# Performance work log

Measured on AMD Instinct MI355X. Metric: run time of the kernel, lower is better.

The kernel has to match this reference:

```python
import jax, jax.numpy as jnp
from jax import lax
import numpy as np

B, S, G = 16, 384, 384
N = S + G
E_CHAR, D = 100, 128
H = D // 2              # LSTM hidden per direction
NHEAD, NHID = 4, 64
T = 21                  # crf_input_dim = label_alphabet.size() + 1
START, STOP = T - 2, T - 1
ALPHA = 0.2
CHAR_V, GAZ_V = 8000, 100000
NEG = -9e15             # pyGAT masked_fill value


def setup_inputs():
    key = jax.random.key(0)
    ks = jax.random.split(key, 20)
    f32 = jnp.float32
    def nrm(k, shape, s=0.05):
        return (jax.random.normal(k, shape) * s).astype(f32)
    eye = jnp.eye(N, dtype=bool)
    def adj(k):
        return ((jax.random.uniform(k, (B, N, N)) < 0.1) | eye[None]).astype(jnp.int32)
    return dict(
        batch_char=jax.random.randint(ks[0], (B, S), 0, CHAR_V),
        batch_len=jnp.full((B,), S, jnp.int32),
        gaz_list=jax.random.randint(ks[1], (B, G), 0, GAZ_V),
        t_graph=adj(ks[2]), c_graph=adj(ks[3]), l_graph=adj(ks[4]),
        mask=jnp.ones((B, S), jnp.int32),
        char_table=nrm(ks[5], (CHAR_V, E_CHAR)),
        gaz_table=nrm(ks[6], (GAZ_V, D)),
        w_ih_f=nrm(ks[7], (4 * H, E_CHAR)), w_hh_f=nrm(ks[8], (4 * H, H)),
        b_f=jnp.zeros((4 * H,), f32),
        w_ih_b=nrm(ks[9], (4 * H, E_CHAR)), w_hh_b=nrm(ks[10], (4 * H, H)),
        b_b=jnp.zeros((4 * H,), f32),
        h2h_W=nrm(ks[11], (T, D)), h2h_b=jnp.zeros((T,), f32),
        gat_Wh=nrm(ks[12], (3, NHEAD, D, NHID)),
        gat_ah=nrm(ks[13], (3, NHEAD, 2 * NHID)),
        gat_Wo=nrm(ks[14], (3, NHEAD * NHID, T)),
        gat_ao=nrm(ks[15], (3, 2 * T)),
        fuse_w=jnp.ones((4,), f32),
        transitions=nrm(ks[16], (T, T)),
    )


def _lstm_dir(x, w_ih, w_hh, b, reverse):
    # x: [B,S,E]; torch gate order i,f,g,o
    Bb = x.shape[0]
    Hh = w_hh.shape[1]
    xw = jnp.einsum('bse,ge->bsg', x, w_ih) + b
    def step(carry, xt):
        h, c = carry
        g = xt + h @ w_hh.T
        i, f, gg, o = jnp.split(g, 4, axis=-1)
        c = jax.nn.sigmoid(f) * c + jax.nn.sigmoid(i) * jnp.tanh(gg)
        h = jax.nn.sigmoid(o) * jnp.tanh(c)
        return (h, c), h
    h0 = jnp.zeros((Bb, Hh), x.dtype)
    _, hs = lax.scan(step, (h0, h0), xw.swapaxes(0, 1), reverse=reverse)
    return hs.swapaxes(0, 1)


def _gat_layer(x, adj, W, a, concat):
    # pyGAT batched layer: e_ij = LeakyReLU(a . [Wh_i || Wh_j]), masked softmax over j
    h = jnp.einsum('bnd,df->bnf', x, W)
    F_ = W.shape[1]
    f1 = h @ a[:F_]           # [B,N]
    f2 = h @ a[F_:]
    e = jax.nn.leaky_relu(f1[:, :, None] + f2[:, None, :], negative_slope=ALPHA)
    e = jnp.where(adj > 0, e, NEG)
    att = jax.nn.softmax(e, axis=-1)
    out = jnp.einsum('bij,bjf->bif', att, h)
    return jax.nn.elu(out) if concat else out


def _gat(x, adj, Wh, ah, Wo, ao):
    heads = jax.vmap(lambda W, a: _gat_layer(x, adj, W, a, True))(Wh, ah)  # [H,B,N,F]
    hcat = jnp.moveaxis(heads, 0, 2).reshape(x.shape[0], x.shape[1], -1)
    return jax.nn.elu(_gat_layer(hcat, adj, Wo, ao, False))


def _crf_feature(batch_char, gaz_list, graphs, char_table, gaz_table,
                 w_ih_f, w_hh_f, b_f, w_ih_b, w_hh_b, b_b, h2h_W, h2h_b,
                 gat_Wh, gat_ah, gat_Wo, gat_ao, fuse_w):
    emb = char_table[batch_char]                      # [B,S,E_CHAR]
    hf = _lstm_dir(emb, w_ih_f, w_hh_f, b_f, False)
    hb = _lstm_dir(emb, w_ih_b, w_hh_b, b_b, True)
    lstm_feat = jnp.concatenate([hf, hb], axis=-1)    # [B,S,D]
    gaz_feat = gaz_table[gaz_list]                    # [B,G,D]
    gat_in = jnp.concatenate([lstm_feat, gaz_feat], axis=1)  # [B,N,D]
    gat_outs = [_gat(gat_in, adj, gat_Wh[k], gat_ah[k], gat_Wo[k], gat_ao[k])[:, :S]
                for k, adj in enumerate(graphs)]
    lstm_proj = lstm_feat @ h2h_W.T + h2h_b           # [B,S,T]
    return (fuse_w[0] * lstm_proj + fuse_w[1] * gat_outs[0]
            + fuse_w[2] * gat_outs[1] + fuse_w[3] * gat_outs[2])


def _viterbi(feats, transitions, mask):
    Bb, Ss, Tt = feats.shape
    ids = jnp.arange(Tt)
    part0 = feats[:, 0, :] + transitions[START][None, :]
    def step(part, inp):
        feat_t, m_t = inp
        cur = part[:, :, None] + transitions[None] + feat_t[:, None, :]  # [B,prev,cur]
        new = cur.max(axis=1)
        bp = cur.argmax(axis=1)
        m = (m_t > 0)[:, None]
        return jnp.where(m, new, part), jnp.where(m, bp, ids[None, :])
    part, bps = lax.scan(step, part0,
                         (feats[:, 1:].swapaxes(0, 1), mask[:, 1:].swapaxes(0, 1)))
    last_tag = jnp.argmax(part + transitions[:, STOP][None, :], axis=1)
    def back(tag, bp):
        prev = jnp.take_along_axis(bp, tag[:, None], axis=1)[:, 0]
        return prev, prev
    _, prevs = lax.scan(back, last_tag, bps, reverse=True)   # prevs[j] = tag at time j
    return jnp.concatenate([prevs.swapaxes(0, 1), last_tag[:, None]], axis=1)


def reference(batch_char, batch_len, gaz_list, t_graph, c_graph, l_graph, mask,
              char_table, gaz_table, w_ih_f, w_hh_f, b_f, w_ih_b, w_hh_b, b_b,
              h2h_W, h2h_b, gat_Wh, gat_ah, gat_Wo, gat_ao, fuse_w, transitions):
    # batch_len is all == S (mask all ones), so packed BiLSTM == plain BiLSTM
    feats = _crf_feature(batch_char, gaz_list, (t_graph, c_graph, l_graph),
                         char_table, gaz_table, w_ih_f, w_hh_f, b_f,
                         w_ih_b, w_hh_b, b_b, h2h_W, h2h_b,
                         gat_Wh, gat_ah, gat_Wo, gat_ao, fuse_w)
    return _viterbi(feats, transitions, mask)
```

## Files before the change

kernel.cpp:

```cpp
#include <hip/hip_runtime.h>
#include <hip/hip_bf16.h>
#include <cstdint>
#include <cstddef>

#define BB 16
#define SS 384
#define GG 384
#define NN 768
#define DD 128
#define EC 100
#define TT 21
#define NHEADS 4
#define BN (BB*NN)
#define BS (BB*SS)

__device__ __forceinline__ float rdlane(float v, int l) {
    return __int_as_float(__builtin_amdgcn_readlane(__float_as_int(v), l));
}
__device__ __forceinline__ float sigf(float x) { return 1.0f / (1.0f + __expf(-x)); }
__device__ __forceinline__ float wred_max(float v) {
    #pragma unroll
    for (int o = 32; o > 0; o >>= 1) v = fmaxf(v, __shfl_xor(v, o));
    return v;
}
__device__ __forceinline__ float wred_sum(float v) {
    #pragma unroll
    for (int o = 32; o > 0; o >>= 1) v += __shfl_xor(v, o);
    return v;
}

__global__ __launch_bounds__(256) void k_xw(
    const int* __restrict__ batch_char, const float* __restrict__ char_table,
    const float* __restrict__ w_ih_f, const float* __restrict__ b_f,
    const float* __restrict__ w_ih_b, const float* __restrict__ b_b,
    float* __restrict__ xw_f, float* __restrict__ xw_b)
{
    __shared__ float At[EC * 68];
    __shared__ float Bt[EC * 68];
    __shared__ int   chs[64];
    const int tid = threadIdx.x;
    const int rt  = blockIdx.x;
    const int ot  = blockIdx.y;
    const int dir = ot >> 2, gt = ot & 3;
    const float* wih  = dir ? w_ih_b : w_ih_f;
    const float* bias = dir ? b_b    : b_f;
    float*       out  = dir ? xw_b   : xw_f;

    if (tid < 64) chs[tid] = batch_char[rt * 64 + tid];
    __syncthreads();
    for (int idx = tid; idx < 64 * EC; idx += 256) {
        int r = idx / EC, e = idx - r * EC;
        At[e * 68 + r] = char_table[(size_t)chs[r] * EC + e];
        Bt[e * 68 + r] = wih[(size_t)(gt * 64 + r) * EC + e];
    }
    __syncthreads();

    const int ty = tid >> 4, tx = tid & 15;
    const int r0 = ty * 4, c0 = tx * 4;
    float acc[4][4] = {};
    #pragma unroll 4
    for (int e = 0; e < EC; ++e) {
        float4 a = *(const float4*)&At[e * 68 + r0];
        float4 bv = *(const float4*)&Bt[e * 68 + c0];
        float av[4] = {a.x, a.y, a.z, a.w};
        float bb[4] = {bv.x, bv.y, bv.z, bv.w};
        #pragma unroll
        for (int i = 0; i < 4; ++i)
            #pragma unroll
            for (int j = 0; j < 4; ++j) acc[i][j] = fmaf(av[i], bb[j], acc[i][j]);
    }
    #pragma unroll
    for (int i = 0; i < 4; ++i) {
        int row = rt * 64 + r0 + i;
        int gc  = gt * 64 + c0;
        float4 o;
        o.x = acc[i][0] + bias[gc + 0];
        o.y = acc[i][1] + bias[gc + 1];
        o.z = acc[i][2] + bias[gc + 2];
        o.w = acc[i][3] + bias[gc + 3];
        *(float4*)&out[(size_t)row * 256 + gc] = o;
    }
}

__global__ __launch_bounds__(256) void k_gaz(
    const int* __restrict__ gaz_list, const float* __restrict__ gaz_table,
    float* __restrict__ gat_in)
{
    int idx = blockIdx.x * 256 + threadIdx.x;
    int d = idx & 127;
    int rest = idx >> 7;
    int g = rest % GG;
    int b = rest / GG;
    float v = gaz_table[(size_t)gaz_list[b * GG + g] * DD + d];
    gat_in[((size_t)b * NN + SS + g) * DD + d] = v;
}

__global__ __launch_bounds__(256) void k_lstm(
    const float* __restrict__ xw_f, const float* __restrict__ xw_b,
    const float* __restrict__ w_hh_f, const float* __restrict__ w_hh_b,
    float* __restrict__ gat_in)
{
    __shared__ float pre[2][256];
    const int tid = threadIdx.x, wave = tid >> 6, lane = tid & 63;
    const int b = blockIdx.x >> 1, dir = blockIdx.x & 1;
    const float* xw = (dir ? xw_b : xw_f) + (size_t)b * SS * 256;
    const float* wrow = (dir ? w_hh_b : w_hh_f) + (size_t)tid * 64;
    float w[64];
    #pragma unroll
    for (int q = 0; q < 16; ++q) {
        float4 v = *(const float4*)&wrow[q * 4];
        w[q * 4 + 0] = v.x; w[q * 4 + 1] = v.y; w[q * 4 + 2] = v.z; w[q * 4 + 3] = v.w;
    }
    float h = 0.f, c = 0.f;
    int buf = 0;
    for (int tt = 0; tt < SS; ++tt) {
        const int t = dir ? (SS - 1 - tt) : tt;
        float pv = xw[t * 256 + tid];
        #pragma unroll
        for (int j = 0; j < 64; ++j) pv = fmaf(rdlane(h, j), w[j], pv);
        pre[buf][lane * 4 + wave] = pv;
        __syncthreads();
        float4 g4 = *(const float4*)&pre[buf][lane * 4];
        float nc = sigf(g4.y) * c + sigf(g4.x) * tanhf(g4.z);
        float nh = sigf(g4.w) * tanhf(nc);
        c = nc; h = nh;
        if (wave == 0) gat_in[((size_t)b * NN + t) * DD + dir * 64 + lane] = h;
        buf ^= 1;
    }
}

__global__ __launch_bounds__(256) void k_p1(
    const float* __restrict__ gat_in, const float* __restrict__ gat_Wh,
    const float* __restrict__ gat_ah, int k,
    float* __restrict__ h1, float* __restrict__ f1g, float* __restrict__ f2g)
{
    __shared__ float At[64 * 68];
    __shared__ float Bt[64 * 68];
    __shared__ float sf1[64], sf2[64];
    const int tid = threadIdx.x;
    const int rt = blockIdx.x, hd = blockIdx.y;
    if (tid < 64) { sf1[tid] = 0.f; sf2[tid] = 0.f; }
    const float* W = gat_Wh + ((size_t)(k * NHEADS + hd)) * DD * 64;
    const int ty = tid >> 4, tx = tid & 15;
    const int r0 = ty * 4, c0 = tx * 4;
    float acc[4][4] = {};
    for (int ph = 0; ph < 2; ++ph) {
        __syncthreads();
        for (int idx = tid; idx < 64 * 64; idx += 256) {
            int r = idx >> 6, e = idx & 63;
            At[e * 68 + r] = gat_in[((size_t)(rt * 64 + r)) * DD + ph * 64 + e];
            int e2 = idx >> 6, f = idx & 63;
            Bt[e2 * 68 + f] = W[(size_t)(ph * 64 + e2) * 64 + f];
        }
        __syncthreads();
        #pragma unroll 4
        for (int e = 0; e < 64; ++e) {
            float4 a = *(const float4*)&At[e * 68 + r0];
            float4 bv = *(const float4*)&Bt[e * 68 + c0];
            float av[4] = {a.x, a.y, a.z, a.w};
            float bb[4] = {bv.x, bv.y, bv.z, bv.w};
            #pragma unroll
            for (int i = 0; i < 4; ++i)
                #pragma unroll
                for (int j = 0; j < 4; ++j) acc[i][j] = fmaf(av[i], bb[j], acc[i][j]);
        }
    }
    const float* ah = gat_ah + (size_t)(k * NHEADS + hd) * 128;
    float a1[4], a2[4];
    #pragma unroll
    for (int j = 0; j < 4; ++j) { a1[j] = ah[c0 + j]; a2[j] = ah[64 + c0 + j]; }
    #pragma unroll
    for (int i = 0; i < 4; ++i) {
        int n = rt * 64 + r0 + i;
        float4 o = make_float4(acc[i][0], acc[i][1], acc[i][2], acc[i][3]);
        *(float4*)&h1[((size_t)n * NHEADS + hd) * 64 + c0] = o;
        float p1 = acc[i][0] * a1[0] + acc[i][1] * a1[1] + acc[i][2] * a1[2] + acc[i][3] * a1[3];
        float p2 = acc[i][0] * a2[0] + acc[i][1] * a2[1] + acc[i][2] * a2[2] + acc[i][3] * a2[3];
        atomicAdd(&sf1[r0 + i], p1);
        atomicAdd(&sf2[r0 + i], p2);
    }
    __syncthreads();
    if (tid < 64) {
        f1g[hd * BN + rt * 64 + tid] = sf1[tid];
        f2g[hd * BN + rt * 64 + tid] = sf2[tid];
    }
}

__global__ __launch_bounds__(256) void k_attn1(
    const int* __restrict__ adj, const float* __restrict__ h1,
    const float* __restrict__ f1g, const float* __restrict__ f2g,
    float* __restrict__ out1, unsigned long long* __restrict__ packed)
{
    __shared__ int   nbr[NN];
    __shared__ float ep[NHEADS][NN];
    __shared__ int   cnt;
    const int tid = threadIdx.x, wave = tid >> 6, lane = tid & 63;
    const int n = blockIdx.x;
    const int b = n / NN;
    if (tid == 0) cnt = 0;
    __syncthreads();
    #pragma unroll
    for (int it = 0; it < 3; ++it) {
        int j = it * 256 + tid;
        int a = adj[(size_t)n * NN + j];
        unsigned long long m = __ballot(a > 0);
        if (lane == 0) packed[(size_t)n * 12 + it * 4 + wave] = m;
        if (a > 0) { int p = atomicAdd(&cnt, 1); nbr[p] = j; }
    }
    __syncthreads();
    const int C = cnt;
    const int hd = wave;
    const float f1 = f1g[hd * BN + n];
    const float* f2p = f2g + hd * BN + b * NN;
    float mx = -3.0e38f;
    for (int t = lane; t < C; t += 64) {
        int j = nbr[t];
        float e = f1 + f2p[j];
        e = (e >= 0.f) ? e : 0.2f * e;
        ep[hd][t] = e;
        mx = fmaxf(mx, e);
    }
    mx = wred_max(mx);
    float sum = 0.f;
    for (int t = lane; t < C; t += 64) {
        float p = __expf(ep[hd][t] - mx);
        ep[hd][t] = p;
        sum += p;
    }
    sum = wred_sum(sum);
    const float* hb = h1 + (size_t)b * NN * (NHEADS * 64) + hd * 64 + lane;
    float acc = 0.f;
    #pragma unroll 4
    for (int t = 0; t < C; ++t) {
        float p = ep[hd][t];
        int j = nbr[t];
        acc = fmaf(p, hb[(size_t)j * (NHEADS * 64)], acc);
    }
    float r = acc / sum;
    r = (r > 0.f) ? r : expm1f(r);
    out1[(size_t)n * 256 + hd * 64 + lane] = r;
}

__global__ __launch_bounds__(256) void k_p2(
    const float* __restrict__ out1, const float* __restrict__ gat_Wo,
    const float* __restrict__ gat_ao, int k,
    float* __restrict__ h2, float* __restrict__ f1o, float* __restrict__ f2o)
{
    __shared__ float ld[12 * 256];
    __shared__ float lf1[12], lf2[12];
    const int tid = threadIdx.x;
    const int blk = blockIdx.x;
    if (tid < 12) { lf1[tid] = 0.f; lf2[tid] = 0.f; }
    for (int idx = tid; idx < 12 * 256; idx += 256)
        ld[idx] = out1[(size_t)blk * 12 * 256 + idx];
    __syncthreads();
    if (tid < 252) {
        const int r = tid / TT, c = tid - r * TT;
        const float* Wo = gat_Wo + (size_t)k * 256 * TT;
        const float4* row4 = (const float4*)&ld[r * 256];
        float acc = 0.f;
        #pragma unroll 8
        for (int q4 = 0; q4 < 64; ++q4) {
            float4 v = row4[q4];
            int q = q4 * 4;
            acc = fmaf(v.x, Wo[(q + 0) * TT + c], acc);
            acc = fmaf(v.y, Wo[(q + 1) * TT + c], acc);
            acc = fmaf(v.z, Wo[(q + 2) * TT + c], acc);
            acc = fmaf(v.w, Wo[(q + 3) * TT + c], acc);
        }
        const int n = blk * 12 + r;
        h2[(size_t)n * TT + c] = acc;
        const float* ao = gat_ao + k * 2 * TT;
        atomicAdd(&lf1[r], acc * ao[c]);
        atomicAdd(&lf2[r], acc * ao[TT + c]);
    }
    __syncthreads();
    if (tid < 12) {
        f1o[blk * 12 + tid] = lf1[tid];
        f2o[blk * 12 + tid] = lf2[tid];
    }
}

__global__ __launch_bounds__(64) void k_attn2(
    const unsigned long long* __restrict__ packed,
    const float* __restrict__ h2, const float* __restrict__ f1o,
    const float* __restrict__ f2o, float* __restrict__ out2k)
{
    __shared__ int   nbr[NN];
    __shared__ float ep[NN];
    const int lane = threadIdx.x;
    const int blk = blockIdx.x;
    const int b = blk / SS, s = blk - b * SS;
    const int n = b * NN + s;
    unsigned long long w64 = (lane < 12) ? packed[(size_t)n * 12 + lane] : 0ULL;
    int pc = __popcll(w64);
    int inc = pc;
    #pragma unroll
    for (int d = 1; d < 16; d <<= 1) {
        int t = __shfl_up(inc, d, 16);
        if ((lane & 15) >= d) inc += t;
    }
    const int C = __shfl(inc, 11);
    int off = inc - pc;
    while (w64) {
        int bit = __builtin_ctzll(w64);
        nbr[off++] = lane * 64 + bit;
        w64 &= w64 - 1;
    }
    __syncthreads();
    const float f1 = f1o[n];
    const float* f2p = f2o + b * NN;
    float mx = -3.0e38f;
    for (int t = lane; t < C; t += 64) {
        int j = nbr[t];
        float e = f1 + f2p[j];
        e = (e >= 0.f) ? e : 0.2f * e;
        ep[t] = e;
        mx = fmaxf(mx, e);
    }
    mx = wred_max(mx);
    float sum = 0.f;
    for (int t = lane; t < C; t += 64) {
        float p = __expf(ep[t] - mx);
        ep[t] = p;
        sum += p;
    }
    sum = wred_sum(sum);
    float acc = 0.f;
    const float* h2b = h2 + (size_t)b * NN * TT + ((lane < TT) ? lane : 0);
    #pragma unroll 4
    for (int t = 0; t < C; ++t) {
        float p = ep[t];
        int j = nbr[t];
        acc = fmaf(p, h2b[(size_t)j * TT], acc);
    }
    if (lane < TT) {
        float r = acc / sum;
        r = (r > 0.f) ? r : expm1f(r);
        out2k[(size_t)blk * TT + lane] = r;
    }
}

__global__ __launch_bounds__(64) void k_fuse(
    const float* __restrict__ gat_in, const float* __restrict__ h2h_W,
    const float* __restrict__ h2h_b, const float* __restrict__ fuse_w,
    const float* __restrict__ out2, float* __restrict__ feats)
{
    __shared__ float row[DD];
    const int lane = threadIdx.x;
    const int blk = blockIdx.x;
    const int b = blk / SS, s = blk - b * SS;
    const float* src = gat_in + ((size_t)b * NN + s) * DD;
    row[lane] = src[lane];
    row[lane + 64] = src[lane + 64];
    __syncthreads();
    if (lane < TT) {
        float acc = h2h_b[lane];
        const float4* w4 = (const float4*)&h2h_W[lane * DD];
        const float4* r4 = (const float4*)row;
        #pragma unroll 8
        for (int d4 = 0; d4 < 32; ++d4) {
            float4 w = w4[d4]; float4 v = r4[d4];
            acc = fmaf(w.x, v.x, acc); acc = fmaf(w.y, v.y, acc);
            acc = fmaf(w.z, v.z, acc); acc = fmaf(w.w, v.w, acc);
        }
        size_t o = (size_t)blk * TT + lane;
        feats[o] = fuse_w[0] * acc + fuse_w[1] * out2[o]
                 + fuse_w[2] * out2[(size_t)BS * TT + o]
                 + fuse_w[3] * out2[2 * (size_t)BS * TT + o];
    }
}

__global__ __launch_bounds__(64) void k_vit(
    const float* __restrict__ feats, const float* __restrict__ trans,
    int* __restrict__ out)
{
    __shared__ float part[24];
    __shared__ unsigned char bp[SS - 1][24];
    const int lane = threadIdx.x;
    const int b = blockIdx.x;
    const int pg = lane / TT;
    const int c = lane - pg * TT;
    const bool act = (pg < 3);
    const int p0 = pg * 7;
    float tc[7];
    if (act) {
        #pragma unroll
        for (int u = 0; u < 7; ++u) tc[u] = trans[(p0 + u) * TT + c];
    }
    if (lane < TT) part[lane] = feats[((size_t)b * SS) * TT + lane] + trans[19 * TT + lane];
    if (lane >= TT && lane < 24) part[lane] = -3.0e38f;
    __syncthreads();
    for (int t = 1; t < SS; ++t) {
        float best = -3.0e38f; int bi = 0;
        if (act) {
            #pragma unroll
            for (int u = 0; u < 7; ++u) {
                float v = part[p0 + u] + tc[u];
                if (v > best) { best = v; bi = p0 + u; }
            }
        }
        float bv1 = __shfl(best, lane + 21);
        int   bi1 = __shfl(bi,   lane + 21);
        float bv2 = __shfl(best, lane + 42);
        int   bi2 = __shfl(bi,   lane + 42);
        if (lane < TT) {
            if (bv1 > best) { best = bv1; bi = bi1; }
            if (bv2 > best) { best = bv2; bi = bi2; }
            bp[t - 1][lane] = (unsigned char)bi;
            part[lane] = best + feats[((size_t)b * SS + t) * TT + lane];
        }
        __syncthreads();
    }
    float fv = (lane < TT) ? part[lane] + trans[lane * TT + 20] : -3.0e38f;
    int fi = (lane < TT) ? lane : 0;
    #pragma unroll
    for (int o = 32; o > 0; o >>= 1) {
        float ov = __shfl_xor(fv, o);
        int oi = __shfl_xor(fi, o);
        if (ov > fv || (ov == fv && oi < fi)) { fv = ov; fi = oi; }
    }
    __syncthreads();
    if (lane == 0) {
        int cur = fi;
        out[b * SS + SS - 1] = cur;
        for (int u = SS - 2; u >= 0; --u) {
            cur = bp[u][cur];
            out[b * SS + u] = cur;
        }
    }
}

extern "C" void kernel_launch(void* const* d_in, const int* in_sizes, int n_in,
                              void* d_out, int out_size, void* d_ws, size_t ws_size,
                              hipStream_t stream) {
    (void)in_sizes; (void)n_in; (void)out_size; (void)ws_size;
    const int*   batch_char = (const int*)d_in[0];
    const int*   gaz_list   = (const int*)d_in[2];
    const int*   graphs[3]  = {(const int*)d_in[3], (const int*)d_in[4], (const int*)d_in[5]};
    const float* char_table = (const float*)d_in[7];
    const float* gaz_table  = (const float*)d_in[8];
    const float* w_ih_f = (const float*)d_in[9];
    const float* w_hh_f = (const float*)d_in[10];
    const float* b_f    = (const float*)d_in[11];
    const float* w_ih_b = (const float*)d_in[12];
    const float* w_hh_b = (const float*)d_in[13];
    const float* b_b    = (const float*)d_in[14];
    const float* h2h_W  = (const float*)d_in[15];
    const float* h2h_b  = (const float*)d_in[16];
    const float* gat_Wh = (const float*)d_in[17];
    const float* gat_ah = (const float*)d_in[18];
    const float* gat_Wo = (const float*)d_in[19];
    const float* gat_ao = (const float*)d_in[20];
    const float* fuse_w = (const float*)d_in[21];
    const float* trans  = (const float*)d_in[22];

    float* ws = (float*)d_ws;
    float* gat_in = ws;
    float* xw_f   = gat_in + 1572864;
    float* xw_b   = xw_f   + 1572864;
    float* h1     = xw_b   + 1572864;
    float* out1   = h1     + 3145728;
    float* h2     = out1   + 3145728;
    float* f1g    = h2     + 258048;
    float* f2g    = f1g    + 49152;
    float* f1o    = f2g    + 49152;
    float* f2o    = f1o    + 12288;
    float* out2   = f2o    + 12288;
    float* feats  = out2   + 387072;
    unsigned long long* packed = (unsigned long long*)(feats + 129024);

    k_xw<<<dim3(96, 8), 256, 0, stream>>>(batch_char, char_table, w_ih_f, b_f,
                                          w_ih_b, b_b, xw_f, xw_b);
    k_gaz<<<3072, 256, 0, stream>>>(gaz_list, gaz_table, gat_in);
    k_lstm<<<32, 256, 0, stream>>>(xw_f, xw_b, w_hh_f, w_hh_b, gat_in);
    for (int k = 0; k < 3; ++k) {
        k_p1<<<dim3(192, 4), 256, 0, stream>>>(gat_in, gat_Wh, gat_ah, k, h1, f1g, f2g);
        k_attn1<<<BN, 256, 0, stream>>>(graphs[k], h1, f1g, f2g, out1, packed);
        k_p2<<<1024, 256, 0, stream>>>(out1, gat_Wo, gat_ao, k, h2, f1o, f2o);
        k_attn2<<<BS, 64, 0, stream>>>(packed, h2, f1o, f2o, out2 + (size_t)k * BS * TT);
    }
    k_fuse<<<BS, 64, 0, stream>>>(gat_in, h2h_W, h2h_b, fuse_w, out2, feats);
    k_vit<<<BB, 64, 0, stream>>>(feats, trans, (int*)d_out);
}
```

Before: 1.039 ms.

## Prefetch LSTM inputs, split FMA chains, deterministic neighbor lists, unroll attention gathers

In the LSTM recurrence, the next step's input projection is prefetched, the 64-term recurrent dot product is split into four independent accumulators, gate values are read from a contiguous shared layout, and tanhf is replaced by an exp-based fast tanh. The GAT attention kernels now build neighbor lists from ballot masks with a prefix sum instead of shared atomics. Their gather-accumulate loops use four independent accumulators to raise memory-level parallelism. The aim is to shorten the serial latency chain in the LSTM and the atomic contention and dependent loads in attention. In exchange, the fast tanh and the reordered sums change floating-point rounding slightly.

```diff
diff --git a/kernel.cpp b/kernel.cpp
--- a/kernel.cpp
+++ b/kernel.cpp
@@ -18,6 +18,9 @@
     return __int_as_float(__builtin_amdgcn_readlane(__float_as_int(v), l));
 }
 __device__ __forceinline__ float sigf(float x) { return 1.0f / (1.0f + __expf(-x)); }
+__device__ __forceinline__ float tanh_fast(float x) {
+    return 1.0f - 2.0f / (__expf(2.0f * x) + 1.0f);
+}
 __device__ __forceinline__ float wred_max(float v) {
     #pragma unroll
     for (int o = 32; o > 0; o >>= 1) v = fmaxf(v, __shfl_xor(v, o));
@@ -113,18 +116,30 @@
     }
     float h = 0.f, c = 0.f;
     int buf = 0;
+    float xv = xw[(dir ? (SS - 1) : 0) * 256 + tid];
     for (int tt = 0; tt < SS; ++tt) {
         const int t = dir ? (SS - 1 - tt) : tt;
-        float pv = xw[t * 256 + tid];
+        const int tn = dir ? (t - 1) : (t + 1);
+        float xnext = (tt + 1 < SS) ? xw[tn * 256 + tid] : 0.f;
+        float a0 = xv, a1 = 0.f, a2 = 0.f, a3 = 0.f;
         #pragma unroll
-        for (int j = 0; j < 64; ++j) pv = fmaf(rdlane(h, j), w[j], pv);
-        pre[buf][lane * 4 + wave] = pv;
+        for (int j = 0; j < 64; j += 4) {
+            a0 = fmaf(rdlane(h, j + 0), w[j + 0], a0);
+            a1 = fmaf(rdlane(h, j + 1), w[j + 1], a1);
+            a2 = fmaf(rdlane(h, j + 2), w[j + 2], a2);
+            a3 = fmaf(rdlane(h, j + 3), w[j + 3], a3);
+        }
+        pre[buf][tid] = (a0 + a1) + (a2 + a3);
         __syncthreads();
-        float4 g4 = *(const float4*)&pre[buf][lane * 4];
-        float nc = sigf(g4.y) * c + sigf(g4.x) * tanhf(g4.z);
-        float nh = sigf(g4.w) * tanhf(nc);
+        float gi = pre[buf][lane];
+        float gf = pre[buf][64 + lane];
+        float gg = pre[buf][128 + lane];
+        float go = pre[buf][192 + lane];
+        float nc = sigf(gf) * c + sigf(gi) * tanh_fast(gg);
+        float nh = sigf(go) * tanh_fast(nc);
         c = nc; h = nh;
         if (wave == 0) gat_in[((size_t)b * NN + t) * DD + dir * 64 + lane] = h;
+        xv = xnext;
         buf ^= 1;
     }
 }
@@ -149,8 +164,7 @@
         for (int idx = tid; idx < 64 * 64; idx += 256) {
             int r = idx >> 6, e = idx & 63;
             At[e * 68 + r] = gat_in[((size_t)(rt * 64 + r)) * DD + ph * 64 + e];
-            int e2 = idx >> 6, f = idx & 63;
-            Bt[e2 * 68 + f] = W[(size_t)(ph * 64 + e2) * 64 + f];
+            Bt[e * 68 + r] = W[(size_t)(ph * 64 + e) * 64 + r];
         }
         __syncthreads();
         #pragma unroll 4
@@ -193,29 +207,42 @@
 {
     __shared__ int   nbr[NN];
     __shared__ float ep[NHEADS][NN];
-    __shared__ int   cnt;
+    __shared__ unsigned long long wm[12];
+    __shared__ int cntS;
     const int tid = threadIdx.x, wave = tid >> 6, lane = tid & 63;
     const int n = blockIdx.x;
     const int b = n / NN;
-    if (tid == 0) cnt = 0;
-    __syncthreads();
     #pragma unroll
     for (int it = 0; it < 3; ++it) {
         int j = it * 256 + tid;
         int a = adj[(size_t)n * NN + j];
         unsigned long long m = __ballot(a > 0);
-        if (lane == 0) packed[(size_t)n * 12 + it * 4 + wave] = m;
-        if (a > 0) { int p = atomicAdd(&cnt, 1); nbr[p] = j; }
-    }
-    __syncthreads();
-    const int C = cnt;
+        if (lane == 0) { wm[it * 4 + wave] = m; packed[(size_t)n * 12 + it * 4 + wave] = m; }
+    }
+    __syncthreads();
+    if (wave == 0) {
+        unsigned long long m = (lane < 12) ? wm[lane] : 0ULL;
+        int pc = __popcll(m);
+        int inc = pc;
+        #pragma unroll
+        for (int d = 1; d < 16; d <<= 1) { int t = __shfl_up(inc, d); if (lane >= d) inc += t; }
+        int C = __shfl(inc, 11);
+        if (lane == 0) cntS = C;
+        int off = inc - pc;
+        while (m) {
+            int bit = __builtin_ctzll(m);
+            nbr[off++] = lane * 64 + bit;
+            m &= m - 1;
+        }
+    }
+    __syncthreads();
+    const int C = cntS;
     const int hd = wave;
     const float f1 = f1g[hd * BN + n];
     const float* f2p = f2g + hd * BN + b * NN;
     float mx = -3.0e38f;
     for (int t = lane; t < C; t += 64) {
-        int j = nbr[t];
-        float e = f1 + f2p[j];
+        float e = f1 + f2p[nbr[t]];
         e = (e >= 0.f) ? e : 0.2f * e;
         ep[hd][t] = e;
         mx = fmaxf(mx, e);
@@ -229,14 +256,18 @@
     }
     sum = wred_sum(sum);
     const float* hb = h1 + (size_t)b * NN * (NHEADS * 64) + hd * 64 + lane;
-    float acc = 0.f;
-    #pragma unroll 4
-    for (int t = 0; t < C; ++t) {
-        float p = ep[hd][t];
-        int j = nbr[t];
-        acc = fmaf(p, hb[(size_t)j * (NHEADS * 64)], acc);
-    }
-    float r = acc / sum;
+    float ac0 = 0.f, ac1 = 0.f, ac2 = 0.f, ac3 = 0.f;
+    int t = 0;
+    for (; t + 3 < C; t += 4) {
+        int j0 = nbr[t], j1 = nbr[t + 1], j2 = nbr[t + 2], j3 = nbr[t + 3];
+        float p0 = ep[hd][t], p1 = ep[hd][t + 1], p2 = ep[hd][t + 2], p3 = ep[hd][t + 3];
+        ac0 = fmaf(p0, hb[(size_t)j0 * 256], ac0);
+        ac1 = fmaf(p1, hb[(size_t)j1 * 256], ac1);
+        ac2 = fmaf(p2, hb[(size_t)j2 * 256], ac2);
+        ac3 = fmaf(p3, hb[(size_t)j3 * 256], ac3);
+    }
+    for (; t < C; ++t) ac0 = fmaf(ep[hd][t], hb[(size_t)nbr[t] * 256], ac0);
+    float r = ((ac0 + ac1) + (ac2 + ac3)) / sum;
     r = (r > 0.f) ? r : expm1f(r);
     out1[(size_t)n * 256 + hd * 64 + lane] = r;
 }
@@ -326,16 +357,20 @@
         sum += p;
     }
     sum = wred_sum(sum);
-    float acc = 0.f;
     const float* h2b = h2 + (size_t)b * NN * TT + ((lane < TT) ? lane : 0);
-    #pragma unroll 4
-    for (int t = 0; t < C; ++t) {
-        float p = ep[t];
-        int j = nbr[t];
-        acc = fmaf(p, h2b[(size_t)j * TT], acc);
-    }
+    float ac0 = 0.f, ac1 = 0.f, ac2 = 0.f, ac3 = 0.f;
+    int t = 0;
+    for (; t + 3 < C; t += 4) {
+        int j0 = nbr[t], j1 = nbr[t + 1], j2 = nbr[t + 2], j3 = nbr[t + 3];
+        float p0 = ep[t], p1 = ep[t + 1], p2 = ep[t + 2], p3 = ep[t + 3];
+        ac0 = fmaf(p0, h2b[(size_t)j0 * TT], ac0);
+        ac1 = fmaf(p1, h2b[(size_t)j1 * TT], ac1);
+        ac2 = fmaf(p2, h2b[(size_t)j2 * TT], ac2);
+        ac3 = fmaf(p3, h2b[(size_t)j3 * TT], ac3);
+    }
+    for (; t < C; ++t) ac0 = fmaf(ep[t], h2b[(size_t)nbr[t] * TT], ac0);
     if (lane < TT) {
-        float r = acc / sum;
+        float r = ((ac0 + ac1) + (ac2 + ac3)) / sum;
         r = (r > 0.f) ? r : expm1f(r);
         out2k[(size_t)blk * TT + lane] = r;
     }
```

Result: faster. 960.7 us (-7.5%).
